# Kernel tuning notes

Hardware: AMD Instinct MI355X
Metric: run time of the kernel (lower is better)

The kernel has to match this reference:

```python
import jax, jax.numpy as jnp
import numpy as np

NSITES = 100000
NYEARS = 20
NVIS = 2
HDIM = 64


def setup_inputs() -> dict:
    key = jax.random.key(0)
    ks = jax.random.split(key, 10)
    def w(k, shape, fan_in):
        return (jax.random.normal(k, shape, jnp.float32) / np.sqrt(fan_in)).astype(jnp.float32)
    return {
        "sxy0": jax.random.normal(ks[0], (1, NSITES, 1), jnp.float32),
        "sxy": jax.random.normal(ks[1], (NSITES, NYEARS - 1, 1), jnp.float32),
        "oxy": jax.random.normal(ks[2], (NSITES, NYEARS, NVIS), jnp.float32),
        # to_h0: Linear(1 -> 64)
        "W_h0": w(ks[3], (HDIM, 1), 1), "b_h0": jnp.zeros((HDIM,), jnp.float32),
        # to_h1: Linear(64 -> 64)
        "W_h1": w(ks[4], (HDIM, HDIM), HDIM), "b_h1": jnp.zeros((HDIM,), jnp.float32),
        # to_hrnn: RNN(input=1, hidden=64, relu)
        "W_ih": w(ks[5], (HDIM, 1), 1), "b_ih": jnp.zeros((HDIM,), jnp.float32),
        "W_hh": w(ks[6], (HDIM, HDIM), HDIM), "b_hh": jnp.zeros((HDIM,), jnp.float32),
        # to_psi0 / to_psi: Linear(64 -> 1)
        "W_psi0": w(ks[7], (1, HDIM), HDIM), "b_psi0": jnp.zeros((1,), jnp.float32),
        "W_psi": w(ks[8], (1, HDIM), HDIM), "b_psi": jnp.zeros((1,), jnp.float32),
        # to_p: Linear(65 -> 1)
        "W_p": w(ks[9], (1, HDIM + 1), HDIM + 1), "b_p": jnp.zeros((1,), jnp.float32),
    }


def reference(sxy0, sxy, oxy, W_h0, b_h0, W_h1, b_h1, W_ih, b_ih, W_hh, b_hh,
              W_psi0, b_psi0, W_psi, b_psi, W_p, b_p):
    # site embeddings -> initial hidden state
    hs = jax.nn.elu(sxy0 @ W_h0.T + b_h0)            # [1, N, H]
    h0 = jax.nn.elu(hs @ W_h1.T + b_h1)              # [1, N, H]

    # single-layer relu RNN, batch_first: sxy [N, T, 1], h0 [1, N, H]
    xs = jnp.swapaxes(sxy, 0, 1)                     # [T, N, 1]
    def step(h, x):
        h_new = jax.nn.relu(x @ W_ih.T + b_ih + h @ W_hh.T + b_hh)
        return h_new, h_new
    _, h_seq = jax.lax.scan(step, h0[0], xs)         # [T, N, H]
    h_out = jnp.swapaxes(h_seq, 0, 1)                # [N, T, H]

    psi0_out = jax.nn.sigmoid(h0 @ W_psi0.T + b_psi0)   # [1, N, 1]
    psi_out = jax.nn.sigmoid(h_out @ W_psi.T + b_psi)   # [N, T, 1]

    # detection prob p[i, t, j] = sigmoid(to_p(cat(H[i, t], oxy[i, t, j])))
    # where H[:, 0] = h0 and H[:, t] = h_out[:, t-1] for t >= 1
    H = jnp.concatenate([h0[0][:, None, :], h_out], axis=1)  # [N, Y, H]
    logits = H @ W_p[:, :HDIM].T + oxy * W_p[0, HDIM] + b_p  # [N, Y, NVIS]
    p = jax.nn.sigmoid(logits)
    return psi0_out, psi_out, p
```

## Files before the change

kernel.cpp:

```cpp
#include <hip/hip_runtime.h>
#include <math.h>

#define NSITES 100000
#define NYEARS 20
#define HDIM 64

typedef __bf16 bf16x8 __attribute__((ext_vector_type(8)));
typedef float f32x4 __attribute__((ext_vector_type(4)));

__device__ __forceinline__ float sigmoidf_(float x) { return 1.0f / (1.0f + __expf(-x)); }
__device__ __forceinline__ float eluf_(float x) { return x > 0.0f ? x : expm1f(x); }

__device__ __forceinline__ bf16x8 cvt8_(const float* p) {
    float4 a = ((const float4*)p)[0];
    float4 b = ((const float4*)p)[1];
    bf16x8 r;
    r[0] = (__bf16)a.x; r[1] = (__bf16)a.y; r[2] = (__bf16)a.z; r[3] = (__bf16)a.w;
    r[4] = (__bf16)b.x; r[5] = (__bf16)b.y; r[6] = (__bf16)b.z; r[7] = (__bf16)b.w;
    return r;
}

__device__ __forceinline__ bf16x8 pack_bf_(f32x4 lo, f32x4 hi) {
    bf16x8 r;
    r[0] = (__bf16)lo[0]; r[1] = (__bf16)lo[1]; r[2] = (__bf16)lo[2]; r[3] = (__bf16)lo[3];
    r[4] = (__bf16)hi[0]; r[5] = (__bf16)hi[1]; r[6] = (__bf16)hi[2]; r[7] = (__bf16)hi[3];
    return r;
}

__global__ __launch_bounds__(64, 3)
void rnet_kernel(const float* __restrict__ sxy0,
                 const float* __restrict__ sxy,
                 const float* __restrict__ oxy,
                 const float* __restrict__ W_h0, const float* __restrict__ b_h0,
                 const float* __restrict__ W_h1, const float* __restrict__ b_h1,
                 const float* __restrict__ W_ih, const float* __restrict__ b_ih,
                 const float* __restrict__ W_hh, const float* __restrict__ b_hh,
                 const float* __restrict__ W_psi0, const float* __restrict__ b_psi0,
                 const float* __restrict__ W_psi, const float* __restrict__ b_psi,
                 const float* __restrict__ W_p, const float* __restrict__ b_p,
                 float* __restrict__ out)
{
    const int lane = threadIdx.x;
    const int s = lane & 15;
    const int q = lane >> 4;
    const int sq = s >> 2, sr = s & 3;
    const int base = blockIdx.x * 16;
    const int site = base + s;

    __shared__ __align__(16) float xs_sh[16 * 19];
    __shared__ __align__(16) float pL_sh[16 * 20];
    __shared__ __align__(16) float psiL_sh[16 * 20];
    __shared__ __align__(16) float psi0L_sh[16];

    float* __restrict__ out_psi0 = out;
    float* __restrict__ out_psi  = out + NSITES;
    float* __restrict__ out_p    = out + 20 * NSITES;

    {
        const float* src = sxy + (size_t)base * (NYEARS - 1);
#pragma unroll
        for (int r = 0; r < 5; ++r) {
            int i = r * 64 + lane;
            if (i < 16 * (NYEARS - 1)) xs_sh[i] = src[i];
        }
    }

    bf16x8 bf[2];
    {
        const float s0v = sxy0[site];
        bf16x8 bf0[2];
#pragma unroll
        for (int kt = 0; kt < 2; ++kt) {
            const float* wp = W_h0 + kt * 32 + q * 8;
            const float* bp = b_h0 + kt * 32 + q * 8;
            float4 w0 = ((const float4*)wp)[0], w1 = ((const float4*)wp)[1];
            float4 c0 = ((const float4*)bp)[0], c1 = ((const float4*)bp)[1];
            float v[8];
            v[0] = eluf_(fmaf(s0v, w0.x, c0.x)); v[1] = eluf_(fmaf(s0v, w0.y, c0.y));
            v[2] = eluf_(fmaf(s0v, w0.z, c0.z)); v[3] = eluf_(fmaf(s0v, w0.w, c0.w));
            v[4] = eluf_(fmaf(s0v, w1.x, c1.x)); v[5] = eluf_(fmaf(s0v, w1.y, c1.y));
            v[6] = eluf_(fmaf(s0v, w1.z, c1.z)); v[7] = eluf_(fmaf(s0v, w1.w, c1.w));
#pragma unroll
            for (int j = 0; j < 8; ++j) bf0[kt][j] = (__bf16)v[j];
        }

        f32x4 acc[4];
#pragma unroll
        for (int mt = 0; mt < 4; ++mt) {
            const int dr = 32 * (mt >> 1) + 8 * q + 4 * (mt & 1);
            float4 b1 = *(const float4*)(b_h1 + dr);
            acc[mt][0] = b1.x; acc[mt][1] = b1.y; acc[mt][2] = b1.z; acc[mt][3] = b1.w;
        }
#pragma unroll
        for (int kt = 0; kt < 2; ++kt)
#pragma unroll
            for (int mt = 0; mt < 4; ++mt) {
                const int ar = 32 * (mt >> 1) + 8 * sq + 4 * (mt & 1) + sr;
                bf16x8 a = cvt8_(W_h1 + ar * 64 + kt * 32 + q * 8);
                acc[mt] = __builtin_amdgcn_mfma_f32_16x16x32_bf16(a, bf0[kt], acc[mt], 0, 0, 0);
            }
        f32x4 e[4];
#pragma unroll
        for (int mt = 0; mt < 4; ++mt)
#pragma unroll
            for (int r = 0; r < 4; ++r) e[mt][r] = eluf_(acc[mt][r]);
        bf[0] = pack_bf_(e[0], e[1]);
        bf[1] = pack_bf_(e[2], e[3]);
    }

    bf16x8 a_hh[4][2];
#pragma unroll
    for (int mt = 0; mt < 4; ++mt) {
        const int ar = 32 * (mt >> 1) + 8 * sq + 4 * (mt & 1) + sr;
#pragma unroll
        for (int kt = 0; kt < 2; ++kt)
            a_hh[mt][kt] = cvt8_(W_hh + ar * 64 + kt * 32 + q * 8);
    }
    bf16x8 a_head[2];
    {
        const float* hrow = (s == 1) ? W_p : ((s == 2) ? W_psi0 : W_psi);
#pragma unroll
        for (int kt = 0; kt < 2; ++kt) a_head[kt] = cvt8_(hrow + kt * 32 + q * 8);
    }
    f32x4 biasD[4], wihD[4];
#pragma unroll
    for (int mt = 0; mt < 4; ++mt) {
        const int dr = 32 * (mt >> 1) + 8 * q + 4 * (mt & 1);
        float4 bi = *(const float4*)(b_ih + dr);
        float4 bh = *(const float4*)(b_hh + dr);
        float4 wi = *(const float4*)(W_ih + dr);
        biasD[mt][0] = bi.x + bh.x; biasD[mt][1] = bi.y + bh.y;
        biasD[mt][2] = bi.z + bh.z; biasD[mt][3] = bi.w + bh.w;
        wihD[mt][0] = wi.x; wihD[mt][1] = wi.y; wihD[mt][2] = wi.z; wihD[mt][3] = wi.w;
    }
    f32x4 headC;
    headC[0] = (q == 0) ? b_psi[0]  : 0.0f;
    headC[1] = (q == 0) ? b_p[0]    : 0.0f;
    headC[2] = (q == 0) ? b_psi0[0] : 0.0f;
    headC[3] = 0.0f;

#pragma unroll 1
    for (int t = 1; t < NYEARS; ++t) {
        const float x = xs_sh[s * 19 + (t - 1)];

        f32x4 acc[4], accH;
#pragma unroll
        for (int mt = 0; mt < 4; ++mt)
            acc[mt] = __builtin_amdgcn_mfma_f32_16x16x32_bf16(a_hh[mt][0], bf[0], biasD[mt], 0, 0, 0);
        accH = __builtin_amdgcn_mfma_f32_16x16x32_bf16(a_head[0], bf[0], headC, 0, 0, 0);
#pragma unroll
        for (int mt = 0; mt < 4; ++mt)
            acc[mt] = __builtin_amdgcn_mfma_f32_16x16x32_bf16(a_hh[mt][1], bf[1], acc[mt], 0, 0, 0);
        accH = __builtin_amdgcn_mfma_f32_16x16x32_bf16(a_head[1], bf[1], accH, 0, 0, 0);

        f32x4 hn[4];
#pragma unroll
        for (int mt = 0; mt < 4; ++mt)
#pragma unroll
            for (int r = 0; r < 4; ++r)
                hn[mt][r] = fmaxf(fmaf(x, wihD[mt][r], acc[mt][r]), 0.0f);
        bf[0] = pack_bf_(hn[0], hn[1]);
        bf[1] = pack_bf_(hn[2], hn[3]);

        if (q == 0) {
            pL_sh[s * 20 + (t - 1)]   = accH[1];
            psiL_sh[s * 20 + (t - 1)] = accH[0];
            if (t == 1) psi0L_sh[s] = accH[2];
        }
    }

    {
        f32x4 accH = __builtin_amdgcn_mfma_f32_16x16x32_bf16(a_head[0], bf[0], headC, 0, 0, 0);
        accH = __builtin_amdgcn_mfma_f32_16x16x32_bf16(a_head[1], bf[1], accH, 0, 0, 0);
        if (q == 0) {
            pL_sh[s * 20 + 19]   = accH[1];
            psiL_sh[s * 20 + 19] = accH[0];
        }
    }

    __syncthreads();

    const float wpo = W_p[HDIM];
    if (lane < 16) out_psi0[base + lane] = sigmoidf_(psi0L_sh[lane]);
#pragma unroll
    for (int r = 0; r < 5; ++r) {
        int i = r * 64 + lane;
        if (i < 16 * 19) {
            int sl = i / 19, c = i - sl * 19;
            out_psi[(size_t)base * 19 + i] = sigmoidf_(psiL_sh[sl * 20 + c + 1]);
        }
    }
    const float4* oxy_b = (const float4*)(oxy + (size_t)base * 40);
    float4* outp_b = (float4*)(out_p + (size_t)base * 40);
#pragma unroll
    for (int r = 0; r < 3; ++r) {
        int i4 = r * 64 + lane;
        if (i4 < 160) {
            float4 ox = oxy_b[i4];
            float lg0 = pL_sh[i4 * 2];
            float lg1 = pL_sh[i4 * 2 + 1];
            float4 pv;
            pv.x = sigmoidf_(fmaf(wpo, ox.x, lg0));
            pv.y = sigmoidf_(fmaf(wpo, ox.y, lg0));
            pv.z = sigmoidf_(fmaf(wpo, ox.z, lg1));
            pv.w = sigmoidf_(fmaf(wpo, ox.w, lg1));
            outp_b[i4] = pv;
        }
    }
}

extern "C" void kernel_launch(void* const* d_in, const int* in_sizes, int n_in,
                              void* d_out, int out_size, void* d_ws, size_t ws_size,
                              hipStream_t stream) {
    const float* sxy0   = (const float*)d_in[0];
    const float* sxy    = (const float*)d_in[1];
    const float* oxy    = (const float*)d_in[2];
    const float* W_h0   = (const float*)d_in[3];
    const float* b_h0   = (const float*)d_in[4];
    const float* W_h1   = (const float*)d_in[5];
    const float* b_h1   = (const float*)d_in[6];
    const float* W_ih   = (const float*)d_in[7];
    const float* b_ih   = (const float*)d_in[8];
    const float* W_hh   = (const float*)d_in[9];
    const float* b_hh   = (const float*)d_in[10];
    const float* W_psi0 = (const float*)d_in[11];
    const float* b_psi0 = (const float*)d_in[12];
    const float* W_psi  = (const float*)d_in[13];
    const float* b_psi  = (const float*)d_in[14];
    const float* W_p    = (const float*)d_in[15];
    const float* b_p    = (const float*)d_in[16];

    float* out = (float*)d_out;

    dim3 block(64);
    dim3 grid(NSITES / 16);
    rnet_kernel<<<grid, block, 0, stream>>>(
        sxy0, sxy, oxy, W_h0, b_h0, W_h1, b_h1, W_ih, b_ih, W_hh, b_hh,
        W_psi0, b_psi0, W_psi, b_psi, W_p, b_p, out);
}
```

Baseline: 149.2 us.

## Stage bf16 weights in LDS and process two waves per block

Blocks now hold two wavefronts of 16 sites each. W_hh and W_h1 are loaded cooperatively once per block, converted to bf16 and stored in padded LDS. Each wave then reads its MFMA A-fragments from LDS instead of doing strided global float loads and per-lane conversion. The W_h1 buffer is reused for the logit staging after a barrier. This halves redundant weight traffic per site, at the cost of more LDS per block, extra barriers and changed occupancy.

```diff
diff --git a/kernel.cpp b/kernel.cpp
--- a/kernel.cpp
+++ b/kernel.cpp
@@ -4,12 +4,19 @@
 #define NSITES 100000
 #define NYEARS 20
 #define HDIM 64
+#define WSTR 72
 
 typedef __bf16 bf16x8 __attribute__((ext_vector_type(8)));
 typedef float f32x4 __attribute__((ext_vector_type(4)));
 
 __device__ __forceinline__ float sigmoidf_(float x) { return 1.0f / (1.0f + __expf(-x)); }
 __device__ __forceinline__ float eluf_(float x) { return x > 0.0f ? x : expm1f(x); }
+
+__device__ __forceinline__ unsigned pack2_(float a, float b) {
+    union { __bf16 h; unsigned short u; } x, y;
+    x.h = (__bf16)a; y.h = (__bf16)b;
+    return ((unsigned)y.u << 16) | (unsigned)x.u;
+}
 
 __device__ __forceinline__ bf16x8 cvt8_(const float* p) {
     float4 a = ((const float4*)p)[0];
@@ -20,6 +27,12 @@
     return r;
 }
 
+__device__ __forceinline__ bf16x8 ldsfrag_(const unsigned short* b, int row, int off) {
+    union { bf16x8 v; uint4 u; } r;
+    r.u = *(const uint4*)&b[row * WSTR + off];
+    return r.v;
+}
+
 __device__ __forceinline__ bf16x8 pack_bf_(f32x4 lo, f32x4 hi) {
     bf16x8 r;
     r[0] = (__bf16)lo[0]; r[1] = (__bf16)lo[1]; r[2] = (__bf16)lo[2]; r[3] = (__bf16)lo[3];
@@ -27,7 +40,7 @@
     return r;
 }
 
-__global__ __launch_bounds__(64, 3)
+__global__ __launch_bounds__(128)
 void rnet_kernel(const float* __restrict__ sxy0,
                  const float* __restrict__ sxy,
                  const float* __restrict__ oxy,
@@ -40,30 +53,50 @@
                  const float* __restrict__ W_p, const float* __restrict__ b_p,
                  float* __restrict__ out)
 {
-    const int lane = threadIdx.x;
+    const int tid  = threadIdx.x;
+    const int lane = tid & 63;
+    const int wv   = tid >> 6;
     const int s = lane & 15;
     const int q = lane >> 4;
     const int sq = s >> 2, sr = s & 3;
-    const int base = blockIdx.x * 16;
-    const int site = base + s;
-
-    __shared__ __align__(16) float xs_sh[16 * 19];
-    __shared__ __align__(16) float pL_sh[16 * 20];
-    __shared__ __align__(16) float psiL_sh[16 * 20];
-    __shared__ __align__(16) float psi0L_sh[16];
+    const int base = blockIdx.x * 32;
+    const int sl   = wv * 16 + s;
+    const int site = base + sl;
+
+    __shared__ __align__(16) unsigned short whh_l[64 * WSTR];
+    __shared__ __align__(16) unsigned short wh1_l[64 * WSTR];
+    __shared__ __align__(16) float xs_sh[32 * 19];
+
+    float* pL    = (float*)wh1_l;
+    float* psiL  = pL + 640;
+    float* psi0L = psiL + 640;
 
     float* __restrict__ out_psi0 = out;
     float* __restrict__ out_psi  = out + NSITES;
     float* __restrict__ out_p    = out + 20 * NSITES;
 
     {
+        const float4* whg = (const float4*)W_hh;
+        const float4* w1g = (const float4*)W_h1;
+#pragma unroll
+        for (int j = 0; j < 8; ++j) {
+            int e4 = j * 128 + tid;
+            int row = e4 >> 4, c4 = e4 & 15;
+            float4 a = whg[e4];
+            uint2 pa; pa.x = pack2_(a.x, a.y); pa.y = pack2_(a.z, a.w);
+            *(uint2*)&whh_l[row * WSTR + c4 * 4] = pa;
+            float4 b = w1g[e4];
+            uint2 pb; pb.x = pack2_(b.x, b.y); pb.y = pack2_(b.z, b.w);
+            *(uint2*)&wh1_l[row * WSTR + c4 * 4] = pb;
+        }
         const float* src = sxy + (size_t)base * (NYEARS - 1);
 #pragma unroll
         for (int r = 0; r < 5; ++r) {
-            int i = r * 64 + lane;
-            if (i < 16 * (NYEARS - 1)) xs_sh[i] = src[i];
-        }
-    }
+            int i = r * 128 + tid;
+            if (i < 32 * (NYEARS - 1)) xs_sh[i] = src[i];
+        }
+    }
+    __syncthreads();
 
     bf16x8 bf[2];
     {
@@ -96,7 +129,7 @@
 #pragma unroll
             for (int mt = 0; mt < 4; ++mt) {
                 const int ar = 32 * (mt >> 1) + 8 * sq + 4 * (mt & 1) + sr;
-                bf16x8 a = cvt8_(W_h1 + ar * 64 + kt * 32 + q * 8);
+                bf16x8 a = ldsfrag_(wh1_l, ar, kt * 32 + q * 8);
                 acc[mt] = __builtin_amdgcn_mfma_f32_16x16x32_bf16(a, bf0[kt], acc[mt], 0, 0, 0);
             }
         f32x4 e[4];
@@ -114,7 +147,7 @@
         const int ar = 32 * (mt >> 1) + 8 * sq + 4 * (mt & 1) + sr;
 #pragma unroll
         for (int kt = 0; kt < 2; ++kt)
-            a_hh[mt][kt] = cvt8_(W_hh + ar * 64 + kt * 32 + q * 8);
+            a_hh[mt][kt] = ldsfrag_(whh_l, ar, kt * 32 + q * 8);
     }
     bf16x8 a_head[2];
     {
@@ -139,9 +172,11 @@
     headC[2] = (q == 0) ? b_psi0[0] : 0.0f;
     headC[3] = 0.0f;
 
+    __syncthreads();
+
 #pragma unroll 1
     for (int t = 1; t < NYEARS; ++t) {
-        const float x = xs_sh[s * 19 + (t - 1)];
+        const float x = xs_sh[sl * 19 + (t - 1)];
 
         f32x4 acc[4], accH;
 #pragma unroll
@@ -163,9 +198,9 @@
         bf[1] = pack_bf_(hn[2], hn[3]);
 
         if (q == 0) {
-            pL_sh[s * 20 + (t - 1)]   = accH[1];
-            psiL_sh[s * 20 + (t - 1)] = accH[0];
-            if (t == 1) psi0L_sh[s] = accH[2];
+            pL[sl * 20 + (t - 1)]   = accH[1];
+            psiL[sl * 20 + (t - 1)] = accH[0];
+            if (t == 1) psi0L[sl] = accH[2];
         }
     }
 
@@ -173,32 +208,32 @@
         f32x4 accH = __builtin_amdgcn_mfma_f32_16x16x32_bf16(a_head[0], bf[0], headC, 0, 0, 0);
         accH = __builtin_amdgcn_mfma_f32_16x16x32_bf16(a_head[1], bf[1], accH, 0, 0, 0);
         if (q == 0) {
-            pL_sh[s * 20 + 19]   = accH[1];
-            psiL_sh[s * 20 + 19] = accH[0];
+            pL[sl * 20 + 19]   = accH[1];
+            psiL[sl * 20 + 19] = accH[0];
         }
     }
 
     __syncthreads();
 
     const float wpo = W_p[HDIM];
-    if (lane < 16) out_psi0[base + lane] = sigmoidf_(psi0L_sh[lane]);
+    if (tid < 32) out_psi0[base + tid] = sigmoidf_(psi0L[tid]);
 #pragma unroll
     for (int r = 0; r < 5; ++r) {
-        int i = r * 64 + lane;
-        if (i < 16 * 19) {
-            int sl = i / 19, c = i - sl * 19;
-            out_psi[(size_t)base * 19 + i] = sigmoidf_(psiL_sh[sl * 20 + c + 1]);
+        int i = r * 128 + tid;
+        if (i < 32 * 19) {
+            int s2 = i / 19, c = i - s2 * 19;
+            out_psi[(size_t)base * 19 + i] = sigmoidf_(psiL[s2 * 20 + c + 1]);
         }
     }
     const float4* oxy_b = (const float4*)(oxy + (size_t)base * 40);
     float4* outp_b = (float4*)(out_p + (size_t)base * 40);
 #pragma unroll
     for (int r = 0; r < 3; ++r) {
-        int i4 = r * 64 + lane;
-        if (i4 < 160) {
+        int i4 = r * 128 + tid;
+        if (i4 < 320) {
             float4 ox = oxy_b[i4];
-            float lg0 = pL_sh[i4 * 2];
-            float lg1 = pL_sh[i4 * 2 + 1];
+            float lg0 = pL[i4 * 2];
+            float lg1 = pL[i4 * 2 + 1];
             float4 pv;
             pv.x = sigmoidf_(fmaf(wpo, ox.x, lg0));
             pv.y = sigmoidf_(fmaf(wpo, ox.y, lg0));
@@ -232,8 +267,8 @@
 
     float* out = (float*)d_out;
 
-    dim3 block(64);
-    dim3 grid(NSITES / 16);
+    dim3 block(128);
+    dim3 grid(NSITES / 32);
     rnet_kernel<<<grid, block, 0, stream>>>(
         sxy0, sxy, oxy, W_h0, b_h0, W_h1, b_h1, W_ih, b_ih, W_hh, b_hh,
         W_psi0, b_psi0, W_psi, b_psi, W_p, b_p, out);
```

After: 144.9 us. -2.8%, faster.
